# Kernel optimization log

Hardware: AMD Instinct MI355X
Metric: run time of the kernel (lower is better)

The kernel has to match this reference:

```python
import jax, jax.numpy as jnp
import numpy as np

B, T, C = 2, 2048, 1024
H, HD = 16, 64
M = 256  # per memory bank
K_CANON = 4


def setup_inputs() -> dict:
    key = jax.random.key(0)
    ks = jax.random.split(key, 10)
    s = 0.02
    return {
        "x": jax.random.normal(ks[0], (B, T, C), jnp.float32),
        "fwd_mem": jax.random.normal(ks[1], (B, M, C), jnp.float32),
        "rev_mem": jax.random.normal(ks[2], (B, M, C), jnp.float32),
        "Wq": jax.random.normal(ks[3], (C, C), jnp.float32) * s,
        "Wk": jax.random.normal(ks[4], (C, C), jnp.float32) * s,
        "Wv": jax.random.normal(ks[5], (C, C), jnp.float32) * s,
        "Wo": jax.random.normal(ks[6], (C, C), jnp.float32) * s,
        "gate_w": jax.random.normal(ks[7], (H, C), jnp.float32) * s,
        "gate_b": jnp.zeros((H,), jnp.float32),
        "canon_w": jax.random.normal(ks[8], (C, 1, K_CANON), jnp.float32) * s,
        "canon_bias": jax.random.normal(ks[9], (C,), jnp.float32) * s,
    }


def _canon_conv(y, canon_w, canon_bias):
    # causal depthwise conv1d with residual; torch weight [C,1,K] -> WIO kernel [K,1,C]
    kern = jnp.transpose(canon_w, (2, 1, 0))
    y_pad = jnp.pad(y, ((0, 0), (K_CANON - 1, 0), (0, 0)))
    conv = jax.lax.conv_general_dilated(
        y_pad, kern, window_strides=(1,), padding='VALID',
        dimension_numbers=('NWC', 'WIO', 'NWC'), feature_group_count=C)
    return y + conv + canon_bias


def reference(x, fwd_mem, rev_mem, Wq, Wk, Wv, Wo, gate_w, gate_b, canon_w, canon_bias):
    Bn, Tn, Cn = x.shape
    scale = 1.0 / np.sqrt(HD)

    q = x @ Wq.T  # [B,T,C]
    k = x @ Wk.T
    v = x @ Wv.T
    # memory integration: project memories with same k/v proj, concat on seq dim
    k = jnp.concatenate([k, fwd_mem @ Wk.T, rev_mem @ Wk.T], axis=1)  # [B,S,C]
    v = jnp.concatenate([v, fwd_mem @ Wv.T, rev_mem @ Wv.T], axis=1)
    S = k.shape[1]
    mem_len = S - Tn

    def heads(t):
        return t.reshape(Bn, -1, H, HD).transpose(0, 2, 1, 3)  # [B,h,S,hd]

    qh, kh, vh = heads(q), heads(k), heads(v)
    scores = jnp.einsum('bhtd,bhsd->bhts', qh, kh) * scale  # [B,h,T,S]
    # causal mask over the first T key columns; memory columns fully visible
    causal = jnp.triu(jnp.ones((Tn, Tn), bool), k=1)
    full_mask = jnp.pad(causal, ((0, 0), (0, mem_len)))  # [T,S]
    scores = jnp.where(full_mask[None, None], -jnp.inf, scores)
    w = jax.nn.softmax(scores, axis=-1)

    # split chunk vs memory, gate memory contribution per head
    w_chunk, w_mem = w[..., :Tn], w[..., Tn:]
    v_chunk, v_mem = vh[:, :, :Tn], vh[:, :, Tn:]
    Y_chunk = jnp.einsum('bhts,bhsd->bhtd', w_chunk, v_chunk)
    Y_mem = jnp.einsum('bhtm,bhmd->bhtd', w_mem, v_mem)
    g = jax.nn.sigmoid(q @ gate_w.T + gate_b)  # [B,T,h]
    g = g.transpose(0, 2, 1)[..., None]  # [B,h,T,1]
    Y = Y_chunk + g * Y_mem

    attn_out = Y.transpose(0, 2, 1, 3).reshape(Bn, Tn, Cn)
    attn_out = _canon_conv(attn_out, canon_w, canon_bias)
    return attn_out @ Wo.T
```

## Files before the change

### kernel.cpp

```cpp
#include <hip/hip_runtime.h>
#include <hip/hip_bf16.h>
#include <cstdint>


typedef __bf16 bf16x8_t __attribute__((ext_vector_type(8)));
typedef __bf16 bf16x4_t __attribute__((ext_vector_type(4)));
typedef float f32x4_t __attribute__((ext_vector_type(4)));

__device__ __forceinline__ f32x4_t mfma16(bf16x8_t a, bf16x8_t b, f32x4_t c) {
    return __builtin_amdgcn_mfma_f32_16x16x32_bf16(a, b, c, 0, 0, 0);
}

__device__ __forceinline__ void gl2lds16(const void* g, void* l) {
    __builtin_amdgcn_global_load_lds(
        (__attribute__((address_space(1))) uint32_t*)(uintptr_t)g,
        (__attribute__((address_space(3))) uint32_t*)l, 16, 0, 0);
}

#define OFF_X   0
#define OFF_FWD 4194304
#define OFF_REV 4718592
#define OFF_WQ  5242880
#define OFF_WK  6291456
#define OFF_WV  7340032
#define OFF_WO  8388608
#define OFF_GW  9437184
#define OFF_GB  9453568
#define OFF_CW  9453584
#define OFF_CB  9457680
#define N_TOT   9458704

__global__ __launch_bounds__(256) void conv_all_kernel(
    const void* p0, const void* p1, const void* p2, const void* p3,
    const void* p4, const void* p5, const void* p6, const void* p7,
    const void* p8, const void* p9, const void* p10,
    __hip_bfloat16* __restrict__ arena)
{
    const int i = (blockIdx.x * 256 + threadIdx.x) * 4;
    if (i >= N_TOT) return;
    const void* src; int off;
    if      (i < OFF_FWD) { src = p0;  off = OFF_X;   }
    else if (i < OFF_REV) { src = p1;  off = OFF_FWD; }
    else if (i < OFF_WQ)  { src = p2;  off = OFF_REV; }
    else if (i < OFF_WK)  { src = p3;  off = OFF_WQ;  }
    else if (i < OFF_WV)  { src = p4;  off = OFF_WK;  }
    else if (i < OFF_WO)  { src = p5;  off = OFF_WV;  }
    else if (i < OFF_GW)  { src = p6;  off = OFF_WO;  }
    else if (i < OFF_GB)  { src = p7;  off = OFF_GW;  }
    else if (i < OFF_CW)  { src = p8;  off = OFF_GB;  }
    else if (i < OFF_CB)  { src = p9;  off = OFF_CW;  }
    else                  { src = p10; off = OFF_CB;  }
    const int j = i - off;
    const float4 f = *(const float4*)((const float*)src + j);
    arena[i + 0] = __float2bfloat16(f.x);
    arena[i + 1] = __float2bfloat16(f.y);
    arena[i + 2] = __float2bfloat16(f.z);
    arena[i + 3] = __float2bfloat16(f.w);
}

__device__ __forceinline__ void gemm_core(
    const __hip_bfloat16* __restrict__ A, const __hip_bfloat16* __restrict__ B,
    void* __restrict__ C, int ldc, int f32o, int arow0, int brow0,
    __hip_bfloat16* As, __hip_bfloat16* Bs)
{
    const int tid  = threadIdx.x;
    const int lane = tid & 63;
    const int wid  = tid >> 6;
    const int q4   = lane >> 4;
    const int c16  = lane & 15;
    const int wm   = (wid >> 1) * 64;
    const int wn   = (wid & 1) * 64;
    const int c0 = tid;
    const int c1 = tid + 256;
    const __hip_bfloat16* gA0 = A + (size_t)(arow0 + (c0 >> 2)) * 1024 + ((c0 & 3) << 3);
    const __hip_bfloat16* gA1 = A + (size_t)(arow0 + (c1 >> 2)) * 1024 + ((c1 & 3) << 3);
    const __hip_bfloat16* gB0 = B + (size_t)(brow0 + (c0 >> 2)) * 1024 + ((c0 & 3) << 3);
    const __hip_bfloat16* gB1 = B + (size_t)(brow0 + (c1 >> 2)) * 1024 + ((c1 & 3) << 3);

    f32x4_t acc[4][4];
#pragma unroll
    for (int i = 0; i < 4; ++i)
#pragma unroll
        for (int j = 0; j < 4; ++j)
#pragma unroll
            for (int r = 0; r < 4; ++r) acc[i][j][r] = 0.0f;

    gl2lds16(gA0, As + c0 * 8);
    gl2lds16(gA1, As + c1 * 8);
    gl2lds16(gB0, Bs + c0 * 8);
    gl2lds16(gB1, Bs + c1 * 8);

    for (int it = 0; it < 32; ++it) {
        __hip_bfloat16* curA = As + (it & 1) * 4096;
        __hip_bfloat16* curB = Bs + (it & 1) * 4096;
        __syncthreads();
        if (it < 31) {
            const int nk = (it + 1) * 32;
            __hip_bfloat16* nA = As + ((it + 1) & 1) * 4096;
            __hip_bfloat16* nB = Bs + ((it + 1) & 1) * 4096;
            gl2lds16(gA0 + nk, nA + c0 * 8);
            gl2lds16(gA1 + nk, nA + c1 * 8);
            gl2lds16(gB0 + nk, nB + c0 * 8);
            gl2lds16(gB1 + nk, nB + c1 * 8);
        }
        bf16x8_t af[4], bfr[4];
#pragma unroll
        for (int i = 0; i < 4; ++i)
            af[i] = *(const bf16x8_t*)&curA[(wm + i * 16 + c16) * 32 + q4 * 8];
#pragma unroll
        for (int j = 0; j < 4; ++j)
            bfr[j] = *(const bf16x8_t*)&curB[(wn + j * 16 + c16) * 32 + q4 * 8];
#pragma unroll
        for (int i = 0; i < 4; ++i)
#pragma unroll
            for (int j = 0; j < 4; ++j)
                acc[i][j] = mfma16(af[i], bfr[j], acc[i][j]);
    }
#pragma unroll
    for (int i = 0; i < 4; ++i) {
        const int mg = arow0 + wm + i * 16 + q4 * 4;
#pragma unroll
        for (int j = 0; j < 4; ++j) {
            const int ng = brow0 + wn + j * 16 + c16;
#pragma unroll
            for (int r = 0; r < 4; ++r) {
                const size_t idx = (size_t)(mg + r) * ldc + ng;
                if (f32o) ((float*)C)[idx] = acc[i][j][r];
                else ((__hip_bfloat16*)C)[idx] = __float2bfloat16(acc[i][j][r]);
            }
        }
    }
}

__global__ __launch_bounds__(256) void qkv_kernel(
    const __hip_bfloat16* __restrict__ x, const __hip_bfloat16* __restrict__ Wqk,
    const __hip_bfloat16* __restrict__ Wv,
    __hip_bfloat16* __restrict__ QK, __hip_bfloat16* __restrict__ Vt)
{
    __shared__ __align__(16) __hip_bfloat16 As[2 * 128 * 32];
    __shared__ __align__(16) __hip_bfloat16 Bs[2 * 128 * 32];
    int id = (blockIdx.x & 7) * 112 + (blockIdx.x >> 3);
    if (id < 512)
        gemm_core(x, Wqk, QK, 2048, 0, (id >> 4) * 128, (id & 15) * 128, As, Bs);
    else if (id < 576) {
        id -= 512;
        gemm_core(x, Wqk, QK, 2048, 0, (32 + (id >> 3)) * 128, (8 + (id & 7)) * 128, As, Bs);
    } else {
        id -= 576;
        gemm_core(Wv, x, Vt, 5120, 0, (id & 7) * 128, (id >> 3) * 128, As, Bs);
    }
}

__global__ __launch_bounds__(256) void gemm_bt_kernel(
    const __hip_bfloat16* __restrict__ A, const __hip_bfloat16* __restrict__ B,
    void* __restrict__ C, int ldc, int f32o)
{
    __shared__ __align__(16) __hip_bfloat16 As[2 * 128 * 32];
    __shared__ __align__(16) __hip_bfloat16 Bs[2 * 128 * 32];
    const int swz = (blockIdx.x & 7) * 32 + (blockIdx.x >> 3);
    const int arow = swz & 31;
    const int brow = swz >> 5;
    gemm_core(A, B, C, ldc, f32o, arow * 128, brow * 128, As, Bs);
}

__global__ __launch_bounds__(64) void gate_kernel(
    const __hip_bfloat16* __restrict__ QK, const __hip_bfloat16* __restrict__ gw,
    const __hip_bfloat16* __restrict__ gb, float* __restrict__ G)
{
    const int base = blockIdx.x * 16;
    const int lane = threadIdx.x;
    const int q4   = lane >> 4;
    const int c16  = lane & 15;
    f32x4_t acc = {0.0f, 0.0f, 0.0f, 0.0f};
    const __hip_bfloat16* qrow = QK + (size_t)(base + c16) * 2048 + q4 * 8;
    const __hip_bfloat16* wrow = gw + (size_t)c16 * 1024 + q4 * 8;
#pragma unroll
    for (int kk = 0; kk < 32; ++kk) {
        const bf16x8_t a = *(const bf16x8_t*)(qrow + kk * 32);
        const bf16x8_t w = *(const bf16x8_t*)(wrow + kk * 32);
        acc = mfma16(a, w, acc);
    }
    const float bias = __bfloat162float(gb[c16]);
#pragma unroll
    for (int r = 0; r < 4; ++r) {
        const int row = base + q4 * 4 + r;
        G[(size_t)row * 16 + c16] = 1.0f / (1.0f + __expf(-(acc[r] + bias)));
    }
}

__global__ __launch_bounds__(256, 4) void attn_kernel(
    const __hip_bfloat16* __restrict__ QK,
    const __hip_bfloat16* __restrict__ Vt,
    const float* __restrict__ G, __hip_bfloat16* __restrict__ Y)
{
    __shared__ __align__(16) __hip_bfloat16 Ks[2][64 * 64];
    __shared__ __align__(16) __hip_bfloat16 Vs[64 * 64];
    __shared__ __align__(16) __hip_bfloat16 Plds[4][16 * 64];
    const int flat = blockIdx.x;
    const int bh   = flat & 31;
    const int tIdx = 31 - (flat >> 5);
    const int b    = bh >> 4;
    const int h    = bh & 15;
    const int tid  = threadIdx.x;
    const int wid  = tid >> 6;
    const int lane = tid & 63;
    const int q4   = lane >> 4;
    const int c16  = lane & 15;
    const int rowbase = tIdx * 64 + wid * 16;

    const __hip_bfloat16* qrow = QK + (size_t)(b * 2048 + rowbase + c16) * 2048 + h * 64;
    const bf16x8_t qa0 = *(const bf16x8_t*)(qrow + q4 * 8);
    const bf16x8_t qa1 = *(const bf16x8_t*)(qrow + 32 + q4 * 8);

    bf16x8_t ones;
#pragma unroll
    for (int i = 0; i < 8; ++i) ones[i] = (__bf16)1.0f;

    float gate[4];
    f32x4_t acc[4];
    f32x4_t rsC = {0.0f, 0.0f, 0.0f, 0.0f};
    f32x4_t rsM = {0.0f, 0.0f, 0.0f, 0.0f};
#pragma unroll
    for (int fp = 0; fp < 4; ++fp)
#pragma unroll
        for (int r = 0; r < 4; ++r) acc[fp][r] = 0.0f;
#pragma unroll
    for (int r = 0; r < 4; ++r)
        gate[r] = G[(size_t)(b * 2048 + rowbase + q4 * 4 + r) * 16 + h];

    const int nCausal = tIdx + 1;
    const int nTiles  = nCausal + 8;
    auto kvRow = [&](int tile) -> int {
        if (tile < nCausal) return b * 2048 + tile * 64;
        const int mi = (tile - nCausal) * 64;
        return (mi < 256) ? 4096 + b * 256 + mi : 4608 + b * 256 + (mi - 256);
    };

    const int srow0 = tid >> 3,         sch0 = (tid & 7) ^ (srow0 & 7);
    const int srow1 = (tid + 256) >> 3, sch1 = (tid & 7) ^ (srow1 & 7);
    const int sw0 = (q4 ^ (c16 & 7)) * 8;
    const int sw1 = ((q4 + 4) ^ (c16 & 7)) * 8;
    const __hip_bfloat16* Kbase = QK + 1024 + h * 64;

    {
        const int vr0 = kvRow(0);
        gl2lds16(Kbase + (size_t)(vr0 + srow0) * 2048 + sch0 * 8, &Ks[0][tid * 8]);
        gl2lds16(Kbase + (size_t)(vr0 + srow1) * 2048 + sch1 * 8, &Ks[0][(tid + 256) * 8]);
    }

    const float SCL = 0.18033688f;

    for (int tile = 0; tile < nTiles; ++tile) {
        const int cur = tile & 1;
        const int vr  = kvRow(tile);
        __syncthreads();
        gl2lds16(Vt + (size_t)(h * 64 + srow0) * 5120 + vr + sch0 * 8, &Vs[tid * 8]);
        gl2lds16(Vt + (size_t)(h * 64 + srow1) * 5120 + vr + sch1 * 8, &Vs[(tid + 256) * 8]);
        __builtin_amdgcn_sched_barrier(0);
        if (tile + 1 < nTiles) {
            const int nr = kvRow(tile + 1);
            gl2lds16(Kbase + (size_t)(nr + srow0) * 2048 + sch0 * 8, &Ks[cur ^ 1][tid * 8]);
            gl2lds16(Kbase + (size_t)(nr + srow1) * 2048 + sch1 * 8, &Ks[cur ^ 1][(tid + 256) * 8]);
        }
        const bool isMem  = (tile >= nCausal);
        const bool isDiag = (tile == nCausal - 1);
        bf16x8_t kb0[4], kb1[4];
#pragma unroll
        for (int f = 0; f < 4; ++f) {
            kb0[f] = *(const bf16x8_t*)&Ks[cur][(f * 16 + c16) * 64 + sw0];
            kb1[f] = *(const bf16x8_t*)&Ks[cur][(f * 16 + c16) * 64 + sw1];
        }
        f32x4_t sc[4];
        __builtin_amdgcn_s_setprio(1);
#pragma unroll
        for (int f = 0; f < 4; ++f) {
            f32x4_t z = {0.0f, 0.0f, 0.0f, 0.0f};
            z = mfma16(qa0, kb0[f], z);
            z = mfma16(qa1, kb1[f], z);
            sc[f] = z;
        }
        __builtin_amdgcn_s_setprio(0);
#pragma unroll
        for (int f = 0; f < 4; ++f)
#pragma unroll
            for (int r = 0; r < 4; ++r) {
                float p = __builtin_amdgcn_exp2f(sc[f][r] * SCL);
                if (isDiag) {
                    const int sg = f * 16 + c16;
                    if (sg > wid * 16 + q4 * 4 + r) p = 0.0f;
                }
                if (isMem) p *= gate[r];
                const int prow = q4 * 4 + r;
                const int pcol = f * 16 + c16;
                Plds[wid][prow * 64 + (((pcol >> 3) ^ (prow & 7)) << 3) + (pcol & 7)] =
                    __float2bfloat16(p);
            }
        if (tile + 1 < nTiles)
            asm volatile("s_waitcnt vmcnt(2) lgkmcnt(0)" ::: "memory");
        else
            asm volatile("s_waitcnt vmcnt(0) lgkmcnt(0)" ::: "memory");
        __builtin_amdgcn_s_barrier();
        __builtin_amdgcn_sched_barrier(0);
        bf16x8_t vb0[4], vb1[4];
#pragma unroll
        for (int f = 0; f < 4; ++f) {
            vb0[f] = *(const bf16x8_t*)&Vs[(f * 16 + c16) * 64 + sw0];
            vb1[f] = *(const bf16x8_t*)&Vs[(f * 16 + c16) * 64 + sw1];
        }
        const bf16x8_t pa0 = *(const bf16x8_t*)&Plds[wid][c16 * 64 + sw0];
        const bf16x8_t pa1 = *(const bf16x8_t*)&Plds[wid][c16 * 64 + sw1];
        __builtin_amdgcn_s_setprio(1);
        if (isMem) {
            rsM = mfma16(pa0, ones, rsM);
            rsM = mfma16(pa1, ones, rsM);
        } else {
            rsC = mfma16(pa0, ones, rsC);
            rsC = mfma16(pa1, ones, rsC);
        }
#pragma unroll
        for (int fp = 0; fp < 4; ++fp) {
            acc[fp] = mfma16(pa0, vb0[fp], acc[fp]);
            acc[fp] = mfma16(pa1, vb1[fp], acc[fp]);
        }
        __builtin_amdgcn_s_setprio(0);
    }

    float inv[4];
#pragma unroll
    for (int r = 0; r < 4; ++r)
        inv[r] = gate[r] / fmaf(gate[r], rsC[r], rsM[r]);
#pragma unroll
    for (int fp = 0; fp < 4; ++fp)
#pragma unroll
        for (int r = 0; r < 4; ++r) {
            const int tg = rowbase + q4 * 4 + r;
            Y[(size_t)(b * 2048 + tg) * 1024 + h * 64 + fp * 16 + c16] =
                __float2bfloat16(acc[fp][r] * inv[r]);
        }
}

__global__ __launch_bounds__(256) void canon_kernel(
    const __hip_bfloat16* __restrict__ Yin, const __hip_bfloat16* __restrict__ cw,
    const __hip_bfloat16* __restrict__ cb, __hip_bfloat16* __restrict__ Yout)
{
    const int gid = blockIdx.x * 256 + threadIdx.x;
    const int cc  = (gid & 255) * 4;
    const int t4  = ((gid >> 8) & 511) * 4;
    const int b   = gid >> 17;
    const size_t base = ((size_t)(b * 2048 + t4)) * 1024 + cc;

    bf16x4_t y[7];
#pragma unroll
    for (int m = 0; m < 7; ++m) {
        if (t4 - 3 + m >= 0)
            y[m] = *(const bf16x4_t*)(Yin + base + (ptrdiff_t)(m - 3) * 1024);
        else {
            y[m][0] = (__bf16)0.0f; y[m][1] = (__bf16)0.0f;
            y[m][2] = (__bf16)0.0f; y[m][3] = (__bf16)0.0f;
        }
    }
    const bf16x8_t w01 = *(const bf16x8_t*)(cw + cc * 4);
    const bf16x8_t w23 = *(const bf16x8_t*)(cw + cc * 4 + 8);
    const bf16x4_t bb  = *(const bf16x4_t*)(cb + cc);

#pragma unroll
    for (int k = 0; k < 4; ++k) {
        float a[4];
#pragma unroll
        for (int i = 0; i < 4; ++i) a[i] = (float)y[k + 3][i] + (float)bb[i];
#pragma unroll
        for (int j = 0; j < 4; ++j) {
            a[0] += (float)y[k + j][0] * (float)w01[j];
            a[1] += (float)y[k + j][1] * (float)w01[4 + j];
            a[2] += (float)y[k + j][2] * (float)w23[j];
            a[3] += (float)y[k + j][3] * (float)w23[4 + j];
        }
        bf16x4_t o;
#pragma unroll
        for (int i = 0; i < 4; ++i) o[i] = (__bf16)a[i];
        *(bf16x4_t*)(Yout + base + (size_t)k * 1024) = o;
    }
}

extern "C" void kernel_launch(void* const* d_in, const int* in_sizes, int n_in,
                              void* d_out, int out_size, void* d_ws, size_t ws_size,
                              hipStream_t stream)
{
    char* ws = (char*)d_ws;
    const size_t MB = 1ull << 20;
    if (ws_size < 50 * MB) return;

    __hip_bfloat16* arena = (__hip_bfloat16*)ws;
    __hip_bfloat16* QK    = (__hip_bfloat16*)(ws + 19 * MB);
    __hip_bfloat16* Vt    = (__hip_bfloat16*)(ws + 39 * MB);
    float*          G     = (float*)(ws + 49 * MB);
    __hip_bfloat16* Y1    = (__hip_bfloat16*)ws;
    __hip_bfloat16* Y2    = QK;

    const dim3 blk(256);
    conv_all_kernel<<<dim3((N_TOT / 4 + 255) / 256), blk, 0, stream>>>(
        d_in[0], d_in[1], d_in[2], d_in[3], d_in[4], d_in[5], d_in[6],
        d_in[7], d_in[8], d_in[9], d_in[10], arena);

    const __hip_bfloat16* xB  = arena + OFF_X;
    const __hip_bfloat16* WqB = arena + OFF_WQ;
    const __hip_bfloat16* WvB = arena + OFF_WV;
    const __hip_bfloat16* WoB = arena + OFF_WO;

    qkv_kernel<<<dim3(896), blk, 0, stream>>>(xB, WqB, WvB, QK, Vt);
    gate_kernel<<<dim3(256), dim3(64), 0, stream>>>(QK, arena + OFF_GW, arena + OFF_GB, G);
    attn_kernel<<<dim3(1024), blk, 0, stream>>>(QK, Vt, G, Y1);
    canon_kernel<<<dim3(1024), blk, 0, stream>>>(Y1, arena + OFF_CW, arena + OFF_CB, Y2);
    gemm_bt_kernel<<<dim3(256), blk, 0, stream>>>(Y2, WoB, d_out, 1024, 1);
}
```

Baseline: 227.2 us.

## Fold gate projection into Wq so gate runs inside the QKV kernel

Precomputes M = gate_w·Wq (16x1024) in extra blocks of the conversion kernel, then computes the gate logits directly from x inside the QKV kernel using 16 extra blocks. This removes the separate gate kernel launch and its dependency on Q having been written. The precompute is a naive fp32 loop over the weights, and the gate now uses a reassociated product rounded to bf16, which slightly changes numerics.

After: 270.3 us. 1.19x slower.

```diff
diff --git a/kernel.cpp b/kernel.cpp
--- a/kernel.cpp
+++ b/kernel.cpp
@@ -29,13 +29,30 @@
 #define OFF_CW  9453584
 #define OFF_CB  9457680
 #define N_TOT   9458704
+#define NB_CONV ((N_TOT / 4 + 255) / 256)
 
 __global__ __launch_bounds__(256) void conv_all_kernel(
     const void* p0, const void* p1, const void* p2, const void* p3,
     const void* p4, const void* p5, const void* p6, const void* p7,
     const void* p8, const void* p9, const void* p10,
-    __hip_bfloat16* __restrict__ arena)
-{
+    __hip_bfloat16* __restrict__ arena, __hip_bfloat16* __restrict__ Mb)
+{
+    if ((int)blockIdx.x >= NB_CONV) {
+        const int mb = blockIdx.x - NB_CONV;
+        const int k  = mb * 16 + (threadIdx.x & 15);
+        const int h  = threadIdx.x >> 4;
+        const float* gwf = (const float*)p7;
+        const float* wqf = (const float*)p3;
+        float acc = 0.0f;
+        for (int c = 0; c < 1024; c += 4) {
+            acc += gwf[h * 1024 + c]     * wqf[(size_t)c * 1024 + k];
+            acc += gwf[h * 1024 + c + 1] * wqf[(size_t)(c + 1) * 1024 + k];
+            acc += gwf[h * 1024 + c + 2] * wqf[(size_t)(c + 2) * 1024 + k];
+            acc += gwf[h * 1024 + c + 3] * wqf[(size_t)(c + 3) * 1024 + k];
+        }
+        Mb[h * 1024 + k] = __float2bfloat16(acc);
+        return;
+    }
     const int i = (blockIdx.x * 256 + threadIdx.x) * 4;
     if (i >= N_TOT) return;
     const void* src; int off;
@@ -135,19 +152,46 @@
 __global__ __launch_bounds__(256) void qkv_kernel(
     const __hip_bfloat16* __restrict__ x, const __hip_bfloat16* __restrict__ Wqk,
     const __hip_bfloat16* __restrict__ Wv,
-    __hip_bfloat16* __restrict__ QK, __hip_bfloat16* __restrict__ Vt)
+    __hip_bfloat16* __restrict__ QK, __hip_bfloat16* __restrict__ Vt,
+    const __hip_bfloat16* __restrict__ Mb, const __hip_bfloat16* __restrict__ gb,
+    float* __restrict__ G)
 {
     __shared__ __align__(16) __hip_bfloat16 As[2 * 128 * 32];
     __shared__ __align__(16) __hip_bfloat16 Bs[2 * 128 * 32];
-    int id = (blockIdx.x & 7) * 112 + (blockIdx.x >> 3);
+    int id = (blockIdx.x & 7) * 114 + (blockIdx.x >> 3);
     if (id < 512)
         gemm_core(x, Wqk, QK, 2048, 0, (id >> 4) * 128, (id & 15) * 128, As, Bs);
     else if (id < 576) {
         id -= 512;
         gemm_core(x, Wqk, QK, 2048, 0, (32 + (id >> 3)) * 128, (8 + (id & 7)) * 128, As, Bs);
-    } else {
+    } else if (id < 896) {
         id -= 576;
         gemm_core(Wv, x, Vt, 5120, 0, (id & 7) * 128, (id >> 3) * 128, As, Bs);
+    } else {
+        const int g    = id - 896;
+        const int tid  = threadIdx.x;
+        const int wid  = tid >> 6;
+        const int lane = tid & 63;
+        const int q4   = lane >> 4;
+        const int c16  = lane & 15;
+        const float gbh = __bfloat162float(gb[c16]);
+        const __hip_bfloat16* mrow = Mb + (size_t)c16 * 1024 + q4 * 8;
+#pragma unroll
+        for (int rt = 0; rt < 4; ++rt) {
+            const int row0 = g * 256 + wid * 64 + rt * 16;
+            const __hip_bfloat16* xrow = x + (size_t)(row0 + c16) * 1024 + q4 * 8;
+            f32x4_t acc = {0.0f, 0.0f, 0.0f, 0.0f};
+#pragma unroll
+            for (int kk = 0; kk < 32; ++kk) {
+                const bf16x8_t a = *(const bf16x8_t*)(xrow + kk * 32);
+                const bf16x8_t m = *(const bf16x8_t*)(mrow + kk * 32);
+                acc = mfma16(a, m, acc);
+            }
+#pragma unroll
+            for (int r = 0; r < 4; ++r)
+                G[(size_t)(row0 + q4 * 4 + r) * 16 + c16] =
+                    1.0f / (1.0f + __expf(-(acc[r] + gbh)));
+        }
     }
 }
 
@@ -161,31 +205,6 @@
     const int arow = swz & 31;
     const int brow = swz >> 5;
     gemm_core(A, B, C, ldc, f32o, arow * 128, brow * 128, As, Bs);
-}
-
-__global__ __launch_bounds__(64) void gate_kernel(
-    const __hip_bfloat16* __restrict__ QK, const __hip_bfloat16* __restrict__ gw,
-    const __hip_bfloat16* __restrict__ gb, float* __restrict__ G)
-{
-    const int base = blockIdx.x * 16;
-    const int lane = threadIdx.x;
-    const int q4   = lane >> 4;
-    const int c16  = lane & 15;
-    f32x4_t acc = {0.0f, 0.0f, 0.0f, 0.0f};
-    const __hip_bfloat16* qrow = QK + (size_t)(base + c16) * 2048 + q4 * 8;
-    const __hip_bfloat16* wrow = gw + (size_t)c16 * 1024 + q4 * 8;
-#pragma unroll
-    for (int kk = 0; kk < 32; ++kk) {
-        const bf16x8_t a = *(const bf16x8_t*)(qrow + kk * 32);
-        const bf16x8_t w = *(const bf16x8_t*)(wrow + kk * 32);
-        acc = mfma16(a, w, acc);
-    }
-    const float bias = __bfloat162float(gb[c16]);
-#pragma unroll
-    for (int r = 0; r < 4; ++r) {
-        const int row = base + q4 * 4 + r;
-        G[(size_t)row * 16 + c16] = 1.0f / (1.0f + __expf(-(acc[r] + bias)));
-    }
 }
 
 __global__ __launch_bounds__(256, 4) void attn_kernel(
@@ -394,21 +413,22 @@
     __hip_bfloat16* QK    = (__hip_bfloat16*)(ws + 19 * MB);
     __hip_bfloat16* Vt    = (__hip_bfloat16*)(ws + 39 * MB);
     float*          G     = (float*)(ws + 49 * MB);
+    __hip_bfloat16* Mb    = (__hip_bfloat16*)(ws + 49 * MB + 512 * 1024);
     __hip_bfloat16* Y1    = (__hip_bfloat16*)ws;
     __hip_bfloat16* Y2    = QK;
 
     const dim3 blk(256);
-    conv_all_kernel<<<dim3((N_TOT / 4 + 255) / 256), blk, 0, stream>>>(
+    conv_all_kernel<<<dim3(NB_CONV + 64), blk, 0, stream>>>(
         d_in[0], d_in[1], d_in[2], d_in[3], d_in[4], d_in[5], d_in[6],
-        d_in[7], d_in[8], d_in[9], d_in[10], arena);
+        d_in[7], d_in[8], d_in[9], d_in[10], arena, Mb);
 
     const __hip_bfloat16* xB  = arena + OFF_X;
     const __hip_bfloat16* WqB = arena + OFF_WQ;
     const __hip_bfloat16* WvB = arena + OFF_WV;
     const __hip_bfloat16* WoB = arena + OFF_WO;
 
-    qkv_kernel<<<dim3(896), blk, 0, stream>>>(xB, WqB, WvB, QK, Vt);
-    gate_kernel<<<dim3(256), dim3(64), 0, stream>>>(QK, arena + OFF_GW, arena + OFF_GB, G);
+    qkv_kernel<<<dim3(912), blk, 0, stream>>>(xB, WqB, WvB, QK, Vt,
+                                              Mb, arena + OFF_GB, G);
     attn_kernel<<<dim3(1024), blk, 0, stream>>>(QK, Vt, G, Y1);
     canon_kernel<<<dim3(1024), blk, 0, stream>>>(Y1, arena + OFF_CW, arena + OFF_CB, Y2);
     gemm_bt_kernel<<<dim3(256), blk, 0, stream>>>(Y2, WoB, d_out, 1024, 1);
```
